# Performance work log

Hardware: AMD Instinct MI355X
Metric: run time of the kernel (lower is better)

## Reference

```python
import jax, jax.numpy as jnp
import numpy as np

LAMBDA_SMOOTHNESS = 1.0
NUM_NODES = 100000
NUM_EDGES = 320000
D_FEAT = 256
NUM_GRAPHS = 128
NUM_CLASSES = 10


def setup_inputs() -> dict:
    key = jax.random.key(0)
    k1, k2, k3, k4, k5 = jax.random.split(key, 5)
    logits = jax.random.normal(k1, (NUM_GRAPHS, NUM_CLASSES), dtype=jnp.float32)
    labels = jax.random.randint(k2, (NUM_GRAPHS,), 0, NUM_CLASSES, dtype=jnp.int64)
    x = jax.random.normal(k3, (NUM_NODES, D_FEAT), dtype=jnp.float32)
    edge_index = jax.random.randint(k4, (2, NUM_EDGES), 0, NUM_NODES, dtype=jnp.int64)
    batch = jnp.sort(jax.random.randint(k5, (NUM_NODES,), 0, NUM_GRAPHS, dtype=jnp.int64))
    return {"logits": logits, "labels": labels, "x": x,
            "edge_index": edge_index, "batch": batch}


def reference(logits, labels, x, edge_index, batch):
    # --- cross entropy over graphs (mean reduction, like F.cross_entropy) ---
    logp = jax.nn.log_softmax(logits, axis=-1)
    ce_loss = -jnp.mean(jnp.take_along_axis(logp, labels[:, None], axis=1))

    # --- Dirichlet smoothness energy, vectorized over all graphs ---
    num_graphs = (jnp.max(batch) + 1).astype(x.dtype)
    row, col = edge_index[0], edge_index[1]
    # edges crossing graph boundaries are dropped by the per-graph edge_mask
    within = (batch[row] == batch[col]).astype(x.dtype)  # [E]
    # per-node degree counting only within-graph edges (== per-graph degree)
    deg = jax.ops.segment_sum(within, row, num_segments=x.shape[0])  # [N]
    deg_inv_sqrt = jnp.where(deg > 0, deg ** -0.5, jnp.zeros_like(deg))
    norm = deg_inv_sqrt[row] * deg_inv_sqrt[col] * within  # [E]
    diff = x[row] - x[col]  # [E, D]
    energy = jnp.sum(norm * jnp.sum(diff * diff, axis=-1))
    smoothness_loss = energy / num_graphs

    return ce_loss + LAMBDA_SMOOTHNESS * smoothness_loss
```

## Files before the change

kernel.cpp:

```cpp
#include <hip/hip_runtime.h>
#include <math.h>

#define CAP 64

__global__ __launch_bounds__(256) void k1_deg_compact_ce(
        const int* __restrict__ row, const int* __restrict__ col,
        const int* __restrict__ batch, unsigned int* __restrict__ deg,
        int2* __restrict__ recs, unsigned int* __restrict__ hcnt, int E,
        const float* __restrict__ logits, const int* __restrict__ labels,
        float* __restrict__ out, int G, int C) {
    __shared__ unsigned int lcnt;
    __shared__ int2 lbuf[CAP];
    if (threadIdx.x == 0) lcnt = 0u;
    __syncthreads();

    int e = blockIdx.x * blockDim.x + threadIdx.x;
    if (e < E) {
        int r = row[e], c = col[e];
        if (batch[r] == batch[c]) {
            atomicAdd(&deg[r], 1u);
            unsigned int idx = atomicAdd(&lcnt, 1u);
            if (idx < CAP) lbuf[idx] = make_int2(r, c);
        }
    }
    __syncthreads();
    unsigned int n = (lcnt < CAP) ? lcnt : CAP;
    if (threadIdx.x < n) recs[(size_t)blockIdx.x * CAP + threadIdx.x] = lbuf[threadIdx.x];
    if (threadIdx.x == 0) hcnt[blockIdx.x] = n;

    if (blockIdx.x == 0) {
        __shared__ float sh[128];
        int g = threadIdx.x;
        if (g < 128) {
            float lp = 0.f;
            if (g < G) {
                const float* lg = logits + (size_t)g * C;
                float m = lg[0];
                for (int d = 1; d < C; ++d) m = fmaxf(m, lg[d]);
                float s = 0.f;
                for (int d = 0; d < C; ++d) s += expf(lg[d] - m);
                lp = lg[labels[g]] - m - logf(s);
            }
            sh[g] = lp;
        }
        __syncthreads();
        for (int o = 64; o > 0; o >>= 1) {
            if (threadIdx.x < o) sh[threadIdx.x] += sh[threadIdx.x + o];
            __syncthreads();
        }
        if (threadIdx.x == 0) out[0] = (float)(-(double)sh[0] / (double)G);
    }
}

__global__ __launch_bounds__(256) void k2_energy(
        const float* __restrict__ x, const unsigned int* __restrict__ deg,
        const int2* __restrict__ recs, const unsigned int* __restrict__ hcnt,
        const int* __restrict__ batch, int N, int nb, int D4,
        float* __restrict__ out) {
    const int lane = threadIdx.x & 63;
    const int wv = threadIdx.x >> 6;
    const int wave = (blockIdx.x * blockDim.x + threadIdx.x) >> 6;

    double wsum = 0.0;
    if (wave < nb) {
        unsigned int n = hcnt[wave];
        for (unsigned int s = 0; s < n; ++s) {
            int2 rc = recs[(size_t)wave * CAP + s];
            unsigned int dr = deg[rc.x];
            unsigned int dc = deg[rc.y];
            if (dc == 0u) continue;
            const float4 a = ((const float4*)(x + (size_t)rc.x * (size_t)(D4 * 4)))[lane];
            const float4 b = ((const float4*)(x + (size_t)rc.y * (size_t)(D4 * 4)))[lane];
            float dx = a.x - b.x, dy = a.y - b.y, dz = a.z - b.z, dw = a.w - b.w;
            float ss = dx * dx + dy * dy + dz * dz + dw * dw;
            #pragma unroll
            for (int o = 32; o > 0; o >>= 1) ss += __shfl_xor(ss, o);
            if (lane == 0) {
                float ir = 1.0f / sqrtf((float)dr);
                float ic = 1.0f / sqrtf((float)dc);
                wsum += (double)((ir * ic) * ss);
            }
        }
    }

    __shared__ double sdw[4];
    if (lane == 0) sdw[wv] = wsum;
    __syncthreads();
    if (threadIdx.x == 0) {
        double bsum = sdw[0] + sdw[1] + sdw[2] + sdw[3];
        if (bsum != 0.0) {
            double ng = (double)(batch[N - 1] + 1);
            atomicAdd(out, (float)(bsum / ng));
        }
    }
}

extern "C" void kernel_launch(void* const* d_in, const int* in_sizes, int n_in,
                              void* d_out, int out_size, void* d_ws, size_t ws_size,
                              hipStream_t stream) {
    const float* logits = (const float*)d_in[0];
    const int* labels = (const int*)d_in[1];
    const float* x = (const float*)d_in[2];
    const int* edge_index = (const int*)d_in[3];
    const int* batch = (const int*)d_in[4];

    const int C = 10;
    const int G = in_sizes[0] / C;
    const int E = in_sizes[3] / 2;
    const int N = in_sizes[4];
    const int D = in_sizes[2] / N;
    const int D4 = D / 4;

    const int* row = edge_index;
    const int* col = edge_index + E;

    int nb = (E + 255) / 256;

    size_t off = 0;
    unsigned int* deg = (unsigned int*)((char*)d_ws + off); off += (size_t)N * 4;
    unsigned int* hcnt = (unsigned int*)((char*)d_ws + off); off += (size_t)nb * 4;
    off = (off + 15) & ~(size_t)15;
    int2* recs = (int2*)((char*)d_ws + off);

    float* out = (float*)d_out;

    hipMemsetAsync(deg, 0, (size_t)N * 4, stream);

    k1_deg_compact_ce<<<nb, 256, 0, stream>>>(row, col, batch, deg, recs, hcnt,
                                              E, logits, labels, out, G, C);

    int k2Blocks = (nb + 3) / 4;
    k2_energy<<<k2Blocks, 256, 0, stream>>>(x, deg, recs, hcnt, batch,
                                            N, nb, D4, out);
}
```

Measured before the change: 21.76 us.

## Replace degree atomics and memset with ballot mask and shared-memory degree counting

```diff
diff --git a/kernel.cpp b/kernel.cpp
--- a/kernel.cpp
+++ b/kernel.cpp
@@ -1,32 +1,25 @@
 #include <hip/hip_runtime.h>
 #include <math.h>
 
-#define CAP 64
+#define RCAP 4096
 
-__global__ __launch_bounds__(256) void k1_deg_compact_ce(
+__global__ __launch_bounds__(256) void k1_mask_ce(
         const int* __restrict__ row, const int* __restrict__ col,
-        const int* __restrict__ batch, unsigned int* __restrict__ deg,
-        int2* __restrict__ recs, unsigned int* __restrict__ hcnt, int E,
+        const int* __restrict__ batch, unsigned long long* __restrict__ mask,
+        int E, int nWords,
         const float* __restrict__ logits, const int* __restrict__ labels,
         float* __restrict__ out, int G, int C) {
-    __shared__ unsigned int lcnt;
-    __shared__ int2 lbuf[CAP];
-    if (threadIdx.x == 0) lcnt = 0u;
-    __syncthreads();
+    int gtid = blockIdx.x * blockDim.x + threadIdx.x;
+    int lane = threadIdx.x & 63;
 
-    int e = blockIdx.x * blockDim.x + threadIdx.x;
-    if (e < E) {
-        int r = row[e], c = col[e];
-        if (batch[r] == batch[c]) {
-            atomicAdd(&deg[r], 1u);
-            unsigned int idx = atomicAdd(&lcnt, 1u);
-            if (idx < CAP) lbuf[idx] = make_int2(r, c);
-        }
+    bool hit = false;
+    if (gtid < E) {
+        int r = row[gtid], c = col[gtid];
+        hit = (batch[r] == batch[c]);
     }
-    __syncthreads();
-    unsigned int n = (lcnt < CAP) ? lcnt : CAP;
-    if (threadIdx.x < n) recs[(size_t)blockIdx.x * CAP + threadIdx.x] = lbuf[threadIdx.x];
-    if (threadIdx.x == 0) hcnt[blockIdx.x] = n;
+    unsigned long long m = __ballot(hit);
+    int w = gtid >> 6;
+    if (lane == 0 && w < nWords) mask[w] = m;
 
     if (blockIdx.x == 0) {
         __shared__ float sh[128];
@@ -35,11 +28,11 @@
             float lp = 0.f;
             if (g < G) {
                 const float* lg = logits + (size_t)g * C;
-                float m = lg[0];
-                for (int d = 1; d < C; ++d) m = fmaxf(m, lg[d]);
+                float mx = lg[0];
+                for (int d = 1; d < C; ++d) mx = fmaxf(mx, lg[d]);
                 float s = 0.f;
-                for (int d = 0; d < C; ++d) s += expf(lg[d] - m);
-                lp = lg[labels[g]] - m - logf(s);
+                for (int d = 0; d < C; ++d) s += expf(lg[d] - mx);
+                lp = lg[labels[g]] - mx - logf(s);
             }
             sh[g] = lp;
         }
@@ -53,24 +46,55 @@
 }
 
 __global__ __launch_bounds__(256) void k2_energy(
-        const float* __restrict__ x, const unsigned int* __restrict__ deg,
-        const int2* __restrict__ recs, const unsigned int* __restrict__ hcnt,
-        const int* __restrict__ batch, int N, int nb, int D4,
-        float* __restrict__ out) {
+        const float* __restrict__ x,
+        const int* __restrict__ row, const int* __restrict__ col,
+        const unsigned long long* __restrict__ mask,
+        const int* __restrict__ batch,
+        float* __restrict__ out, int nWords, int wpb, int D4, int N) {
+    __shared__ int rrows[RCAP];
+    __shared__ unsigned int lcnt;
+    if (threadIdx.x == 0) lcnt = 0u;
+    __syncthreads();
+
+    for (int w = threadIdx.x; w < nWords; w += blockDim.x) {
+        unsigned long long m = mask[w];
+        while (m) {
+            int bit = __ffsll(m) - 1;
+            m &= m - 1;
+            unsigned int idx = atomicAdd(&lcnt, 1u);
+            if (idx < RCAP) rrows[idx] = row[w * 64 + bit];
+        }
+    }
+    __syncthreads();
+    int cnt = (lcnt < RCAP) ? (int)lcnt : RCAP;
+
     const int lane = threadIdx.x & 63;
     const int wv = threadIdx.x >> 6;
-    const int wave = (blockIdx.x * blockDim.x + threadIdx.x) >> 6;
+    int w0 = blockIdx.x * wpb;
+    int w1 = (w0 + wpb < nWords) ? (w0 + wpb) : nWords;
 
     double wsum = 0.0;
-    if (wave < nb) {
-        unsigned int n = hcnt[wave];
-        for (unsigned int s = 0; s < n; ++s) {
-            int2 rc = recs[(size_t)wave * CAP + s];
-            unsigned int dr = deg[rc.x];
-            unsigned int dc = deg[rc.y];
-            if (dc == 0u) continue;
-            const float4 a = ((const float4*)(x + (size_t)rc.x * (size_t)(D4 * 4)))[lane];
-            const float4 b = ((const float4*)(x + (size_t)rc.y * (size_t)(D4 * 4)))[lane];
+    for (int w = w0 + wv; w < w1; w += 4) {
+        unsigned long long m = mask[w];
+        while (m) {
+            int bit = __ffsll(m) - 1;
+            m &= m - 1;
+            int e = w * 64 + bit;
+            int r = row[e], c = col[e];
+            int cr = 0, cc = 0;
+            for (int i = lane; i < cnt; i += 64) {
+                int v = rrows[i];
+                cr += (v == r);
+                cc += (v == c);
+            }
+            int packed = cr | (cc << 16);
+            #pragma unroll
+            for (int o = 32; o > 0; o >>= 1) packed += __shfl_xor(packed, o);
+            int dr = packed & 0xffff;
+            int dc = packed >> 16;
+            if (dc == 0) continue;
+            const float4 a = ((const float4*)(x + (size_t)r * (size_t)(D4 * 4)))[lane];
+            const float4 b = ((const float4*)(x + (size_t)c * (size_t)(D4 * 4)))[lane];
             float dx = a.x - b.x, dy = a.y - b.y, dz = a.z - b.z, dw = a.w - b.w;
             float ss = dx * dx + dy * dy + dz * dz + dw * dw;
             #pragma unroll
@@ -114,22 +138,17 @@
     const int* row = edge_index;
     const int* col = edge_index + E;
 
-    int nb = (E + 255) / 256;
+    int nWords = (E + 63) / 64;
 
-    size_t off = 0;
-    unsigned int* deg = (unsigned int*)((char*)d_ws + off); off += (size_t)N * 4;
-    unsigned int* hcnt = (unsigned int*)((char*)d_ws + off); off += (size_t)nb * 4;
-    off = (off + 15) & ~(size_t)15;
-    int2* recs = (int2*)((char*)d_ws + off);
-
+    unsigned long long* mask = (unsigned long long*)d_ws;
     float* out = (float*)d_out;
 
-    hipMemsetAsync(deg, 0, (size_t)N * 4, stream);
+    int k1Blocks = (E + 255) / 256;
+    k1_mask_ce<<<k1Blocks, 256, 0, stream>>>(row, col, batch, mask, E, nWords,
+                                             logits, labels, out, G, C);
 
-    k1_deg_compact_ce<<<nb, 256, 0, stream>>>(row, col, batch, deg, recs, hcnt,
-                                              E, logits, labels, out, G, C);
-
-    int k2Blocks = (nb + 3) / 4;
-    k2_energy<<<k2Blocks, 256, 0, stream>>>(x, deg, recs, hcnt, batch,
-                                            N, nb, D4, out);
+    int k2Blocks = 125;
+    int wpb = (nWords + k2Blocks - 1) / k2Blocks;
+    k2_energy<<<k2Blocks, 256, 0, stream>>>(x, row, col, mask, batch, out,
+                                            nWords, wpb, D4, N);
 }
```

New measurement: 63.82 us. 2.93x slower.
